# Optimization experiments

Hardware: AMD Instinct MI355X
Metric: run time of the kernel (lower is better)

Reference implementation:

```python
import jax, jax.numpy as jnp
import numpy as np
import math
from jax import lax


def _conv1d(x, w, stride=1):
    """Cross-correlation (torch F.conv1d semantics), VALID. x:[B,L], w:[K] -> [B,Lout]."""
    out = lax.conv_general_dilated(
        x[:, None, :], w[None, None, :], window_strides=(stride,), padding='VALID',
        dimension_numbers=('NCH', 'OIH', 'NCH'))
    return out[:, 0, :]


def setup_inputs() -> dict:
    B, D, K, NS = 32768, 1024, 8, 10  # batch, dim, filter_length, num_sparse_params
    key = jax.random.key(0)
    k_x, k_lo, k_hi, k_sp = jax.random.split(key, 4)
    x = jax.random.normal(k_x, (B, D), dtype=jnp.float32)
    sqrt2 = math.sqrt(2.0)
    base_lo = jnp.array([1.0, 1.0], dtype=jnp.float32) / sqrt2
    base_hi = jnp.array([1.0, -1.0], dtype=jnp.float32) / sqrt2
    dec_lo = jnp.pad(base_lo, (0, K - 2)) + 0.01 * jax.random.normal(k_lo, (K,), jnp.float32)
    dec_hi = jnp.pad(base_hi, (0, K - 2)) + 0.01 * jax.random.normal(k_hi, (K,), jnp.float32)
    rec_lo = dec_lo  # cloned from dec at init
    rec_hi = dec_hi
    std = math.sqrt(2.0 / D)
    sparse_coeffs = std * jax.random.normal(k_sp, (NS,), jnp.float32)
    # distinct indices from randperm(dim), all < 2*coeff_len so all valid
    sparse_indices = jnp.asarray(np.random.default_rng(0).permutation(D)[:NS], dtype=jnp.int32)
    return {"x": x, "dec_lo": dec_lo, "dec_hi": dec_hi, "rec_lo": rec_lo,
            "rec_hi": rec_hi, "sparse_coeffs": sparse_coeffs,
            "sparse_indices": sparse_indices}


def reference(x, dec_lo, dec_hi, rec_lo, rec_hi, sparse_coeffs, sparse_indices):
    B, D = x.shape
    K = dec_lo.shape[0]
    p = K - 1  # reflect pad size = 7
    # ---- DWT: reflect pad, correlate with flipped dec filters, stride-2 downsample ----
    xp = jnp.pad(x, ((0, 0), (p, p)), mode='reflect')          # [B, D+14]
    lo = _conv1d(xp, dec_lo[::-1], stride=2)                   # [B, 516]
    hi = _conv1d(xp, dec_hi[::-1], stride=2)                   # [B, 516]
    Lc = lo.shape[1]
    # ---- sparse coefficient injection at fixed indices (distinct indices) ----
    flat = jnp.concatenate([lo, hi], axis=1)                   # [B, 2*Lc]
    flat = flat.at[:, sparse_indices].add(sparse_coeffs[None, :])
    lo2, hi2 = flat[:, :Lc], flat[:, Lc:2 * Lc]
    # ---- IDWT: zero-upsample, reflect pad, correlate with rec filters ----
    up_lo = jnp.zeros((B, 2 * Lc), x.dtype).at[:, ::2].set(lo2)
    up_hi = jnp.zeros((B, 2 * Lc), x.dtype).at[:, ::2].set(hi2)
    up_lo = jnp.pad(up_lo, ((0, 0), (p, p)), mode='reflect')
    up_hi = jnp.pad(up_hi, ((0, 0), (p, p)), mode='reflect')
    rec = _conv1d(up_lo, rec_lo) + _conv1d(up_hi, rec_hi)      # [B, 2*Lc + p] = [B, 1039]
    rec = rec[:, :D]                                           # crop to target length (1039 > 1024)
    return x + rec
```

## Files before the change

kernel.cpp:

```cpp
#include <hip/hip_runtime.h>

#define D_LEN 1024
#define K_LEN 8
#define PAD   7
#define LC    516
#define NS    10

typedef float floatx4 __attribute__((ext_vector_type(4)));

__global__ __launch_bounds__(256) void wavecore_kernel(
    const float* __restrict__ x,
    const float* __restrict__ dec_lo, const float* __restrict__ dec_hi,
    const float* __restrict__ rec_lo, const float* __restrict__ rec_hi,
    const float* __restrict__ sp_c,   const int* __restrict__ sp_i,
    float* __restrict__ out)
{
    __shared__ __align__(16) float  sx[D_LEN];
    __shared__ __align__(16) float2 st[512];

    const int tid = threadIdx.x;
    const size_t rowoff = (size_t)blockIdx.x * D_LEN;

    floatx4 xv = __builtin_nontemporal_load(((const floatx4*)(x + rowoff)) + tid);
    ((floatx4*)sx)[tid] = xv;

    float f_dlo[K_LEN], f_dhi[K_LEN], f_rlo[K_LEN], f_rhi[K_LEN];
#pragma unroll
    for (int k = 0; k < K_LEN; ++k) {
        f_dlo[k] = dec_lo[k];
        f_dhi[k] = dec_hi[k];
        f_rlo[k] = rec_lo[k];
        f_rhi[k] = rec_hi[k];
    }
    __syncthreads();

    float lo0 = 0.f, hi0 = 0.f, lo1 = 0.f, hi1 = 0.f;
    if (tid >= 2) {
        const float4 wa = ((const float4*)sx)[tid - 2];
        const float4 wb = ((const float4*)sx)[tid - 1];
        const float w[12] = { wa.x, wa.y, wa.z, wa.w,
                              wb.x, wb.y, wb.z, wb.w,
                              xv.x, xv.y, xv.z, xv.w };
#pragma unroll
        for (int j = 0; j < K_LEN; ++j) {
            const float v0 = w[8  - j];
            const float v1 = w[10 - j];
            lo0 = fmaf(v0, f_dlo[j], lo0);
            hi0 = fmaf(v0, f_dhi[j], hi0);
            lo1 = fmaf(v1, f_dlo[j], lo1);
            hi1 = fmaf(v1, f_dhi[j], hi1);
        }
    } else {
#pragma unroll
        for (int q = 0; q < 2; ++q) {
            const int c = 2 * tid + q;
            float aL = 0.f, aH = 0.f;
#pragma unroll
            for (int j = 0; j < K_LEN; ++j) {
                int m = 2 * c - j;
                m = (m < 0) ? -m : m;
                const float v = sx[m];
                aL = fmaf(v, f_dlo[j], aL);
                aH = fmaf(v, f_dhi[j], aH);
            }
            if (q == 0) { lo0 = aL; hi0 = aH; }
            else        { lo1 = aL; hi1 = aH; }
        }
    }
    {
        float4 pr;
        pr.x = lo0; pr.y = hi0; pr.z = lo1; pr.w = hi1;
        ((float4*)st)[tid] = pr;
    }
    __syncthreads();

    if (tid < NS) {
        const int s = sp_i[tid];
        const float v = sp_c[tid];
        if (s < 512)            st[s].x       += v;
        else if (s >= LC)       st[s - LC].y  += v;
    }
    __syncthreads();

    float res0, res1, res2, res3;
    if (tid >= 2) {
        const float4 qa = ((const float4*)st)[tid - 2];
        const float4 qb = ((const float4*)st)[tid - 1];
        const float4 qc = ((const float4*)st)[tid];
        const float p0l = qa.z, p0h = qa.w;
        const float p1l = qb.x, p1h = qb.y;
        const float p2l = qb.z, p2h = qb.w;
        const float p3l = qc.x, p3h = qc.y;
        const float p4l = qc.z, p4h = qc.w;
        res0 = p0l*f_rlo[1] + p0h*f_rhi[1] + p1l*f_rlo[3] + p1h*f_rhi[3]
             + p2l*f_rlo[5] + p2h*f_rhi[5] + p3l*f_rlo[7] + p3h*f_rhi[7];
        res1 = p0l*f_rlo[0] + p0h*f_rhi[0] + p1l*f_rlo[2] + p1h*f_rhi[2]
             + p2l*f_rlo[4] + p2h*f_rhi[4] + p3l*f_rlo[6] + p3h*f_rhi[6];
        res2 = p1l*f_rlo[1] + p1h*f_rhi[1] + p2l*f_rlo[3] + p2h*f_rhi[3]
             + p3l*f_rlo[5] + p3h*f_rhi[5] + p4l*f_rlo[7] + p4h*f_rhi[7];
        res3 = p1l*f_rlo[0] + p1h*f_rhi[0] + p2l*f_rlo[2] + p2h*f_rhi[2]
             + p3l*f_rlo[4] + p3h*f_rhi[4] + p4l*f_rlo[6] + p4h*f_rhi[6];
    } else {
        float acc[4];
#pragma unroll
        for (int j = 0; j < 4; ++j) {
            const int t  = 4 * tid + j;
            const int k0 = ((j & 1) ^ 1);
            float a = 0.f;
#pragma unroll
            for (int i = 0; i < 4; ++i) {
                const int k = k0 + 2 * i;
                int m = t + k - PAD;
                m = (m < 0) ? -m : m;
                const float2 pv = st[m >> 1];
                a = fmaf(pv.x, f_rlo[k], a);
                a = fmaf(pv.y, f_rhi[k], a);
            }
            acc[j] = a;
        }
        res0 = acc[0]; res1 = acc[1]; res2 = acc[2]; res3 = acc[3];
    }

    floatx4 r;
    r.x = res0 + xv.x;
    r.y = res1 + xv.y;
    r.z = res2 + xv.z;
    r.w = res3 + xv.w;
    __builtin_nontemporal_store(r, ((floatx4*)(out + rowoff)) + tid);
}

extern "C" void kernel_launch(void* const* d_in, const int* in_sizes, int n_in,
                              void* d_out, int out_size, void* d_ws, size_t ws_size,
                              hipStream_t stream) {
    const float* x      = (const float*)d_in[0];
    const float* dec_lo = (const float*)d_in[1];
    const float* dec_hi = (const float*)d_in[2];
    const float* rec_lo = (const float*)d_in[3];
    const float* rec_hi = (const float*)d_in[4];
    const float* sp_c   = (const float*)d_in[5];
    const int*   sp_i   = (const int*)d_in[6];
    float* out = (float*)d_out;

    const int Brows = in_sizes[0] / D_LEN;
    wavecore_kernel<<<Brows, 256, 0, stream>>>(x, dec_lo, dec_hi, rec_lo, rec_hi,
                                               sp_c, sp_i, out);
}
```

Baseline: 56.31 us.

## Use persistent grid with prefetched rows and precomputed sparse-injection delta

The sparse-coefficient injection is linear, so its contribution to the output is computed once in a tiny pre-kernel into workspace and added per row. The main kernel switches to a fixed grid of 2048 blocks, each looping over rows with double-buffered shared memory and register prefetch two rows ahead. The IDWT reuses the thread's own DWT results from registers instead of reading them back from shared memory. This adds a second launch, drops the nontemporal load/store hints, and assumes the row count divides evenly by the grid size.

```diff
diff --git a/kernel.cpp b/kernel.cpp
--- a/kernel.cpp
+++ b/kernel.cpp
@@ -2,83 +2,30 @@
 
 #define D_LEN 1024
 #define K_LEN 8
-#define PAD   7
-#define LC    516
 #define NS    10
-
-typedef float floatx4 __attribute__((ext_vector_type(4)));
-
-__global__ __launch_bounds__(256) void wavecore_kernel(
-    const float* __restrict__ x,
-    const float* __restrict__ dec_lo, const float* __restrict__ dec_hi,
+#define LCC   516
+#define GRID  2048
+
+__global__ __launch_bounds__(256) void wave_delta(
     const float* __restrict__ rec_lo, const float* __restrict__ rec_hi,
     const float* __restrict__ sp_c,   const int* __restrict__ sp_i,
-    float* __restrict__ out)
+    float* __restrict__ delta)
 {
-    __shared__ __align__(16) float  sx[D_LEN];
     __shared__ __align__(16) float2 st[512];
-
     const int tid = threadIdx.x;
-    const size_t rowoff = (size_t)blockIdx.x * D_LEN;
-
-    floatx4 xv = __builtin_nontemporal_load(((const floatx4*)(x + rowoff)) + tid);
-    ((floatx4*)sx)[tid] = xv;
-
-    float f_dlo[K_LEN], f_dhi[K_LEN], f_rlo[K_LEN], f_rhi[K_LEN];
-#pragma unroll
-    for (int k = 0; k < K_LEN; ++k) {
-        f_dlo[k] = dec_lo[k];
-        f_dhi[k] = dec_hi[k];
-        f_rlo[k] = rec_lo[k];
-        f_rhi[k] = rec_hi[k];
-    }
+
+    float frl[K_LEN], frh[K_LEN];
+#pragma unroll
+    for (int k = 0; k < K_LEN; ++k) { frl[k] = rec_lo[k]; frh[k] = rec_hi[k]; }
+
+    float4 z; z.x = 0.f; z.y = 0.f; z.z = 0.f; z.w = 0.f;
+    ((float4*)st)[tid] = z;
     __syncthreads();
-
-    float lo0 = 0.f, hi0 = 0.f, lo1 = 0.f, hi1 = 0.f;
-    if (tid >= 2) {
-        const float4 wa = ((const float4*)sx)[tid - 2];
-        const float4 wb = ((const float4*)sx)[tid - 1];
-        const float w[12] = { wa.x, wa.y, wa.z, wa.w,
-                              wb.x, wb.y, wb.z, wb.w,
-                              xv.x, xv.y, xv.z, xv.w };
-#pragma unroll
-        for (int j = 0; j < K_LEN; ++j) {
-            const float v0 = w[8  - j];
-            const float v1 = w[10 - j];
-            lo0 = fmaf(v0, f_dlo[j], lo0);
-            hi0 = fmaf(v0, f_dhi[j], hi0);
-            lo1 = fmaf(v1, f_dlo[j], lo1);
-            hi1 = fmaf(v1, f_dhi[j], hi1);
-        }
-    } else {
-#pragma unroll
-        for (int q = 0; q < 2; ++q) {
-            const int c = 2 * tid + q;
-            float aL = 0.f, aH = 0.f;
-#pragma unroll
-            for (int j = 0; j < K_LEN; ++j) {
-                int m = 2 * c - j;
-                m = (m < 0) ? -m : m;
-                const float v = sx[m];
-                aL = fmaf(v, f_dlo[j], aL);
-                aH = fmaf(v, f_dhi[j], aH);
-            }
-            if (q == 0) { lo0 = aL; hi0 = aH; }
-            else        { lo1 = aL; hi1 = aH; }
-        }
-    }
-    {
-        float4 pr;
-        pr.x = lo0; pr.y = hi0; pr.z = lo1; pr.w = hi1;
-        ((float4*)st)[tid] = pr;
-    }
-    __syncthreads();
-
     if (tid < NS) {
         const int s = sp_i[tid];
         const float v = sp_c[tid];
-        if (s < 512)            st[s].x       += v;
-        else if (s >= LC)       st[s - LC].y  += v;
+        if (s < 512)       st[s].x = v;
+        else if (s >= LCC) st[s - LCC].y = v;
     }
     __syncthreads();
 
@@ -92,14 +39,14 @@
         const float p2l = qb.z, p2h = qb.w;
         const float p3l = qc.x, p3h = qc.y;
         const float p4l = qc.z, p4h = qc.w;
-        res0 = p0l*f_rlo[1] + p0h*f_rhi[1] + p1l*f_rlo[3] + p1h*f_rhi[3]
-             + p2l*f_rlo[5] + p2h*f_rhi[5] + p3l*f_rlo[7] + p3h*f_rhi[7];
-        res1 = p0l*f_rlo[0] + p0h*f_rhi[0] + p1l*f_rlo[2] + p1h*f_rhi[2]
-             + p2l*f_rlo[4] + p2h*f_rhi[4] + p3l*f_rlo[6] + p3h*f_rhi[6];
-        res2 = p1l*f_rlo[1] + p1h*f_rhi[1] + p2l*f_rlo[3] + p2h*f_rhi[3]
-             + p3l*f_rlo[5] + p3h*f_rhi[5] + p4l*f_rlo[7] + p4h*f_rhi[7];
-        res3 = p1l*f_rlo[0] + p1h*f_rhi[0] + p2l*f_rlo[2] + p2h*f_rhi[2]
-             + p3l*f_rlo[4] + p3h*f_rhi[4] + p4l*f_rlo[6] + p4h*f_rhi[6];
+        res0 = p0l*frl[1] + p0h*frh[1] + p1l*frl[3] + p1h*frh[3]
+             + p2l*frl[5] + p2h*frh[5] + p3l*frl[7] + p3h*frh[7];
+        res1 = p0l*frl[0] + p0h*frh[0] + p1l*frl[2] + p1h*frh[2]
+             + p2l*frl[4] + p2h*frh[4] + p3l*frl[6] + p3h*frh[6];
+        res2 = p1l*frl[1] + p1h*frh[1] + p2l*frl[3] + p2h*frh[3]
+             + p3l*frl[5] + p3h*frh[5] + p4l*frl[7] + p4h*frh[7];
+        res3 = p1l*frl[0] + p1h*frh[0] + p2l*frl[2] + p2h*frh[2]
+             + p3l*frl[4] + p3h*frh[4] + p4l*frl[6] + p4h*frh[6];
     } else {
         float acc[4];
 #pragma unroll
@@ -110,23 +57,143 @@
 #pragma unroll
             for (int i = 0; i < 4; ++i) {
                 const int k = k0 + 2 * i;
-                int m = t + k - PAD;
+                int m = t + k - 7;
                 m = (m < 0) ? -m : m;
                 const float2 pv = st[m >> 1];
-                a = fmaf(pv.x, f_rlo[k], a);
-                a = fmaf(pv.y, f_rhi[k], a);
+                a = fmaf(pv.x, frl[k], a);
+                a = fmaf(pv.y, frh[k], a);
             }
             acc[j] = a;
         }
         res0 = acc[0]; res1 = acc[1]; res2 = acc[2]; res3 = acc[3];
     }
-
-    floatx4 r;
-    r.x = res0 + xv.x;
-    r.y = res1 + xv.y;
-    r.z = res2 + xv.z;
-    r.w = res3 + xv.w;
-    __builtin_nontemporal_store(r, ((floatx4*)(out + rowoff)) + tid);
+    float4 r; r.x = res0; r.y = res1; r.z = res2; r.w = res3;
+    ((float4*)delta)[tid] = r;
+}
+
+__global__ __launch_bounds__(256) void wavecore_kernel(
+    const float* __restrict__ x,
+    const float* __restrict__ dec_lo, const float* __restrict__ dec_hi,
+    const float* __restrict__ rec_lo, const float* __restrict__ rec_hi,
+    const float* __restrict__ delta,
+    float* __restrict__ out, int J)
+{
+    __shared__ __align__(16) float  sx[2][D_LEN];
+    __shared__ __align__(16) float2 st[512];
+
+    const int tid = threadIdx.x;
+
+    float fdl[K_LEN], fdh[K_LEN], frl[K_LEN], frh[K_LEN];
+#pragma unroll
+    for (int k = 0; k < K_LEN; ++k) {
+        fdl[k] = dec_lo[k]; fdh[k] = dec_hi[k];
+        frl[k] = rec_lo[k]; frh[k] = rec_hi[k];
+    }
+    const float4 dq = ((const float4*)delta)[tid];
+
+    size_t off = (size_t)blockIdx.x * D_LEN + 4 * (size_t)tid;
+    const size_t rstride = (size_t)GRID * D_LEN;
+    float4 xv = *(const float4*)(x + off);
+    ((float4*)sx[0])[tid] = xv;
+    float4 xn;
+    { xn = *(const float4*)(x + off + rstride); }
+    __syncthreads();
+
+    int cur = 0;
+#pragma unroll 1
+    for (int j = 0; j < J; ++j) {
+        float4 xn2;
+        if (j + 2 < J) xn2 = *(const float4*)(x + off + 2 * rstride);
+
+        const float* sxc = sx[cur];
+        float lo0 = 0.f, hi0 = 0.f, lo1 = 0.f, hi1 = 0.f;
+        if (tid >= 2) {
+            const float4 wa = ((const float4*)sxc)[tid - 2];
+            const float4 wb = ((const float4*)sxc)[tid - 1];
+            const float w[12] = { wa.x, wa.y, wa.z, wa.w,
+                                  wb.x, wb.y, wb.z, wb.w,
+                                  xv.x, xv.y, xv.z, xv.w };
+#pragma unroll
+            for (int jj = 0; jj < K_LEN; ++jj) {
+                const float v0 = w[8  - jj];
+                const float v1 = w[10 - jj];
+                lo0 = fmaf(v0, fdl[jj], lo0);
+                hi0 = fmaf(v0, fdh[jj], hi0);
+                lo1 = fmaf(v1, fdl[jj], lo1);
+                hi1 = fmaf(v1, fdh[jj], hi1);
+            }
+        } else {
+#pragma unroll
+            for (int q = 0; q < 2; ++q) {
+                const int c = 2 * tid + q;
+                float aL = 0.f, aH = 0.f;
+#pragma unroll
+                for (int jj = 0; jj < K_LEN; ++jj) {
+                    int m = 2 * c - jj;
+                    m = (m < 0) ? -m : m;
+                    const float v = sxc[m];
+                    aL = fmaf(v, fdl[jj], aL);
+                    aH = fmaf(v, fdh[jj], aH);
+                }
+                if (q == 0) { lo0 = aL; hi0 = aH; }
+                else        { lo1 = aL; hi1 = aH; }
+            }
+        }
+        {
+            float4 pr; pr.x = lo0; pr.y = hi0; pr.z = lo1; pr.w = hi1;
+            ((float4*)st)[tid] = pr;
+        }
+        if (j + 1 < J) ((float4*)sx[cur ^ 1])[tid] = xn;
+        __syncthreads();
+
+        float res0, res1, res2, res3;
+        if (tid >= 2) {
+            const float4 qa = ((const float4*)st)[tid - 2];
+            const float4 qb = ((const float4*)st)[tid - 1];
+            const float p0l = qa.z, p0h = qa.w;
+            const float p1l = qb.x, p1h = qb.y;
+            const float p2l = qb.z, p2h = qb.w;
+            const float p3l = lo0,  p3h = hi0;
+            const float p4l = lo1,  p4h = hi1;
+            res0 = p0l*frl[1] + p0h*frh[1] + p1l*frl[3] + p1h*frh[3]
+                 + p2l*frl[5] + p2h*frh[5] + p3l*frl[7] + p3h*frh[7];
+            res1 = p0l*frl[0] + p0h*frh[0] + p1l*frl[2] + p1h*frh[2]
+                 + p2l*frl[4] + p2h*frh[4] + p3l*frl[6] + p3h*frh[6];
+            res2 = p1l*frl[1] + p1h*frh[1] + p2l*frl[3] + p2h*frh[3]
+                 + p3l*frl[5] + p3h*frh[5] + p4l*frl[7] + p4h*frh[7];
+            res3 = p1l*frl[0] + p1h*frh[0] + p2l*frl[2] + p2h*frh[2]
+                 + p3l*frl[4] + p3h*frh[4] + p4l*frl[6] + p4h*frh[6];
+        } else {
+            float acc[4];
+#pragma unroll
+            for (int jj = 0; jj < 4; ++jj) {
+                const int t  = 4 * tid + jj;
+                const int k0 = ((jj & 1) ^ 1);
+                float a = 0.f;
+#pragma unroll
+                for (int i = 0; i < 4; ++i) {
+                    const int k = k0 + 2 * i;
+                    int m = t + k - 7;
+                    m = (m < 0) ? -m : m;
+                    const float2 pv = st[m >> 1];
+                    a = fmaf(pv.x, frl[k], a);
+                    a = fmaf(pv.y, frh[k], a);
+                }
+                acc[jj] = a;
+            }
+            res0 = acc[0]; res1 = acc[1]; res2 = acc[2]; res3 = acc[3];
+        }
+
+        float4 r;
+        r.x = res0 + xv.x + dq.x;
+        r.y = res1 + xv.y + dq.y;
+        r.z = res2 + xv.z + dq.z;
+        r.w = res3 + xv.w + dq.w;
+        *(float4*)(out + off) = r;
+        __syncthreads();
+
+        xv = xn; xn = xn2; cur ^= 1; off += rstride;
+    }
 }
 
 extern "C" void kernel_launch(void* const* d_in, const int* in_sizes, int n_in,
@@ -139,9 +206,13 @@
     const float* rec_hi = (const float*)d_in[4];
     const float* sp_c   = (const float*)d_in[5];
     const int*   sp_i   = (const int*)d_in[6];
-    float* out = (float*)d_out;
+    float* out   = (float*)d_out;
+    float* delta = (float*)d_ws;
 
     const int Brows = in_sizes[0] / D_LEN;
-    wavecore_kernel<<<Brows, 256, 0, stream>>>(x, dec_lo, dec_hi, rec_lo, rec_hi,
-                                               sp_c, sp_i, out);
+    const int J     = Brows / GRID;
+
+    wave_delta<<<1, 256, 0, stream>>>(rec_lo, rec_hi, sp_c, sp_i, delta);
+    wavecore_kernel<<<GRID, 256, 0, stream>>>(x, dec_lo, dec_hi, rec_lo, rec_hi,
+                                              delta, out, J);
 }
```

Result: faster. 49.48 us (-12.1%).
